# Performance work log

Measured on AMD Instinct MI355X. Metric: run time of the kernel, lower is better.

## Reference

```python
import jax, jax.numpy as jnp
import numpy as np


def setup_inputs() -> dict:
    key = jax.random.key(0)
    ks = jax.random.split(key, 7)
    B, S, E = 2, 4096, 512
    return {
        "query": jax.random.normal(ks[0], (B, S, E), jnp.float32),
        "key": jax.random.normal(ks[1], (B, S, E), jnp.float32),
        "value": jax.random.normal(ks[2], (B, S, E), jnp.float32),
        "in_proj_weight": jax.random.normal(ks[3], (3 * E, E), jnp.float32) * 0.02,
        "in_proj_bias": jax.random.normal(ks[4], (3 * E,), jnp.float32) * 0.02,
        "out_proj_weight": jax.random.normal(ks[5], (E, E), jnp.float32) * 0.02,
        "out_proj_bias": jax.random.normal(ks[6], (E,), jnp.float32) * 0.02,
        "window_size": 512,
        "stride": 256,
    }


def reference(query, key, value, in_proj_weight, in_proj_bias,
              out_proj_weight, out_proj_bias, window_size, stride):
    B, S, E = query.shape
    H = 8
    hd = E // H
    scale = 1.0 / np.sqrt(hd).astype(np.float32)

    # Project full sequences once (equivalent to projecting each window slice).
    wq, wk, wv = in_proj_weight[:E], in_proj_weight[E:2 * E], in_proj_weight[2 * E:]
    bq, bk, bv = in_proj_bias[:E], in_proj_bias[E:2 * E], in_proj_bias[2 * E:]
    qp = query @ wq.T + bq   # [B,S,E]
    kp = key @ wk.T + bk
    vp = value @ wv.T + bv

    # Overlapping window gather: [nw, W] token indices.
    starts = np.arange(0, S - window_size + 1, stride)
    idx = starts[:, None] + np.arange(window_size)[None, :]  # [nw, W]
    nw, W = idx.shape

    def heads(x):  # [B,S,E] -> [B,nw,W,H,hd]
        return x[:, idx].reshape(B, nw, W, H, hd)

    qh, kh, vh = heads(qp), heads(kp), heads(vp)

    scores = jnp.einsum('bnqhd,bnkhd->bnhqk', qh, kh) * scale  # [B,nw,H,W,W]
    probs = jax.nn.softmax(scores, axis=-1)
    ctx = jnp.einsum('bnhqk,bnkhd->bnqhd', probs, vh)           # [B,nw,W,H,hd]
    ctx = ctx.reshape(B, nw * W, E)                             # concat over windows
    return ctx @ out_proj_weight.T + out_proj_bias              # [B, nw*W, E]
```

## Files before the change

### kernel.cpp

```cpp
#include <hip/hip_runtime.h>
#include <hip/hip_bf16.h>

typedef __bf16 bf16x8 __attribute__((ext_vector_type(8)));
typedef float f32x4 __attribute__((ext_vector_type(4)));
typedef float f32x16 __attribute__((ext_vector_type(16)));

__device__ __forceinline__ ushort f2bf(float f) {
  union { float f; unsigned u; } x; x.f = f;
  unsigned r = x.u + 0x7fffu + ((x.u >> 16) & 1u);
  return (ushort)(r >> 16);
}

__device__ __forceinline__ void gld_lds16(const void* g, void* l) {
  __builtin_amdgcn_global_load_lds(
      (const __attribute__((address_space(1))) void*)g,
      (__attribute__((address_space(3))) void*)l, 16, 0, 0);
}

__global__ __launch_bounds__(256) void k_cvt_all(
    const float* __restrict__ q, const float* __restrict__ k,
    const float* __restrict__ v, const float* __restrict__ wi,
    const float* __restrict__ wo, ushort* __restrict__ dst) {
  const int NQ = 1048576;
  const int NWI = 196608, NWO = 65536;
  const int total = 3 * NQ + NWI + NWO;
  int i = blockIdx.x * 256 + threadIdx.x;
  int stride = gridDim.x * 256;
  for (; i < total; i += stride) {
    const float* s; int j;
    if (i < NQ)              { s = q;  j = i; }
    else if (i < 2 * NQ)     { s = k;  j = i - NQ; }
    else if (i < 3 * NQ)     { s = v;  j = i - 2 * NQ; }
    else if (i < 3 * NQ + NWI) { s = wi; j = i - 3 * NQ; }
    else                     { s = wo; j = i - 3 * NQ - NWI; }
    float4 val = reinterpret_cast<const float4*>(s)[j];
    ushort4 o;
    o.x = f2bf(val.x); o.y = f2bf(val.y); o.z = f2bf(val.z); o.w = f2bf(val.w);
    reinterpret_cast<ushort4*>(dst)[i] = o;
  }
}

#define GK 512
#define GN 512

__global__ __launch_bounds__(256) void k_gemm(
    const ushort* __restrict__ Abase, size_t az,
    const ushort* __restrict__ Btbase, size_t bz,
    const float* __restrict__ biasbase, int biz,
    void* __restrict__ Cbase, size_t cz,
    int out_bf16, float qs)
{
  int z = blockIdx.z;
  const ushort* A  = Abase  + az * z;
  const ushort* Bt = Btbase + bz * z;
  const float* bias = biasbase + (size_t)biz * z;
  float osc = (z == 0) ? qs : 1.0f;

  __shared__ ushort As[128 * 32];
  __shared__ ushort Bs[128 * 32];

  int tid = threadIdx.x;
  int wv = tid >> 6, ln = tid & 63;
  int l15 = ln & 15, lg = ln >> 4;
  int wm = wv >> 1, wn = wv & 1;
  int m0 = blockIdx.x * 128, n0 = blockIdx.y * 128;

  f32x4 acc[4][4] = {};

  for (int kt = 0; kt < GK / 32; ++kt) {
    __syncthreads();
#pragma unroll
    for (int h2 = 0; h2 < 2; ++h2) {
      int c = h2 * 256 + wv * 64 + ln;
      int row = c >> 2, kc = (c & 3) * 8;
      gld_lds16(A  + (size_t)(m0 + row) * GK + kt * 32 + kc,
                (char*)As + (h2 * 256 + wv * 64) * 16);
      gld_lds16(Bt + (size_t)(n0 + row) * GK + kt * 32 + kc,
                (char*)Bs + (h2 * 256 + wv * 64) * 16);
    }
    __syncthreads();
    bf16x8 af[4], bf[4];
#pragma unroll
    for (int mf = 0; mf < 4; ++mf)
      af[mf] = *reinterpret_cast<const bf16x8*>(&As[(wm * 64 + mf * 16 + l15) * 32 + lg * 8]);
#pragma unroll
    for (int nf = 0; nf < 4; ++nf)
      bf[nf] = *reinterpret_cast<const bf16x8*>(&Bs[(wn * 64 + nf * 16 + l15) * 32 + lg * 8]);
#pragma unroll
    for (int mf = 0; mf < 4; ++mf)
#pragma unroll
      for (int nf = 0; nf < 4; ++nf)
        acc[mf][nf] = __builtin_amdgcn_mfma_f32_16x16x32_bf16(af[mf], bf[nf], acc[mf][nf], 0, 0, 0);
  }

#pragma unroll
  for (int mf = 0; mf < 4; ++mf)
#pragma unroll
    for (int nf = 0; nf < 4; ++nf)
#pragma unroll
      for (int r = 0; r < 4; ++r) {
        int rr = m0 + wm * 64 + mf * 16 + lg * 4 + r;
        int cc = n0 + wn * 64 + nf * 16 + l15;
        float v = (acc[mf][nf][r] + bias[cc]) * osc;
        if (out_bf16)
          ((ushort*)Cbase + cz * z)[(size_t)rr * GN + cc] = f2bf(v);
        else
          ((float*)Cbase)[(size_t)rr * GN + cc] = v;
      }
}

__global__ __launch_bounds__(512, 4) void k_attn(
    const ushort* __restrict__ qp, const ushort* __restrict__ kp,
    const ushort* __restrict__ vp, ushort* __restrict__ ctx)
{
  const int E = 512, SEQ = 4096;
  int bid = blockIdx.x;
  int qh = bid & 1;
  int h = (bid >> 1) & 7;
  int n = (bid >> 4) % 15;
  int b = bid / 240;
  int start = n * 256;

  int tid = threadIdx.x;
  int w = tid >> 6, ln = tid & 63;
  int l31 = ln & 31, hi = ln >> 5;

  size_t base = ((size_t)(b * SEQ + start)) * E + h * 64;
  const ushort* Kw = kp + base;
  const ushort* Vw = vp + base;
  const ushort* Qw = qp + base;

  __shared__ ushort Vt[32768];

  {
    const ushort* src = Vw + (size_t)tid * E;
    uint4 rowv[8];
#pragma unroll
    for (int i = 0; i < 8; ++i)
      rowv[i] = reinterpret_cast<const uint4*>(src)[i];
    const uint* rw = (const uint*)rowv;
    char* lbw = (char*)Vt;
    int kb2 = tid * 2;
#pragma unroll
    for (int d = 0; d < 64; ++d) {
      uint vv = rw[d >> 1];
      ushort e = (d & 1) ? (ushort)(vv >> 16) : (ushort)(vv & 0xffffu);
      int off = d * 1024 + (kb2 ^ ((d & 7) << 4));
      *(ushort*)(lbw + off) = e;
    }
  }
  __syncthreads();

  int q0 = qh * 256 + w * 32;

  bf16x8 qf[4];
#pragma unroll
  for (int i = 0; i < 4; ++i)
    qf[i] = *reinterpret_cast<const bf16x8*>(
        Qw + (size_t)(q0 + l31) * E + i * 16 + hi * 8);

  f32x16 c0 = {}, c1 = {};
  float psum = 0.f;
  const char* lb = (const char*)Vt;

#pragma unroll 2
  for (int kb = 0; kb < 16; ++kb) {
    bf16x8 kf[4];
#pragma unroll
    for (int i = 0; i < 4; ++i)
      kf[i] = *reinterpret_cast<const bf16x8*>(
          Kw + (size_t)(kb * 32 + l31) * E + i * 16 + hi * 8);

    f32x16 s = {};
    __builtin_amdgcn_s_setprio(1);
#pragma unroll
    for (int i = 0; i < 4; ++i)
      s = __builtin_amdgcn_mfma_f32_32x32x16_bf16(kf[i], qf[i], s, 0, 0, 0);
    __builtin_amdgcn_s_setprio(0);

#pragma unroll
    for (int r = 0; r < 16; ++r) {
      float e = __builtin_amdgcn_exp2f(s[r]);
      s[r] = e;
      psum += e;
    }

    uint cw[8];
#pragma unroll
    for (int i = 0; i < 8; ++i)
      asm("v_cvt_pk_bf16_f32 %0, %1, %2"
          : "=v"(cw[i]) : "v"(s[2 * i]), "v"(s[2 * i + 1]));
    asm volatile("v_permlane32_swap_b32 %0, %1" : "+v"(cw[0]), "+v"(cw[2]));
    asm volatile("v_permlane32_swap_b32 %0, %1" : "+v"(cw[1]), "+v"(cw[3]));
    asm volatile("v_permlane32_swap_b32 %0, %1" : "+v"(cw[4]), "+v"(cw[6]));
    asm volatile("v_permlane32_swap_b32 %0, %1" : "+v"(cw[5]), "+v"(cw[7]));
    union { uint u[4]; bf16x8 v; } A1, A2;
    A1.u[0] = cw[0]; A1.u[1] = cw[1]; A1.u[2] = cw[2]; A1.u[3] = cw[3];
    A2.u[0] = cw[4]; A2.u[1] = cw[5]; A2.u[2] = cw[6]; A2.u[3] = cw[7];

    bf16x8 vb00, vb01, vb10, vb11;
    {
      int row = l31, rowh = 32 + l31;
      int cb0 = kb * 64 + hi * 16;
      int cb1 = cb0 + 32;
      vb00 = *reinterpret_cast<const bf16x8*>(lb + row * 1024 + (cb0 ^ ((row & 7) << 4)));
      vb01 = *reinterpret_cast<const bf16x8*>(lb + rowh * 1024 + (cb0 ^ ((row & 7) << 4)));
      vb10 = *reinterpret_cast<const bf16x8*>(lb + row * 1024 + (cb1 ^ ((row & 7) << 4)));
      vb11 = *reinterpret_cast<const bf16x8*>(lb + rowh * 1024 + (cb1 ^ ((row & 7) << 4)));
    }
    __builtin_amdgcn_s_setprio(1);
    c0 = __builtin_amdgcn_mfma_f32_32x32x16_bf16(A1.v, vb00, c0, 0, 0, 0);
    c1 = __builtin_amdgcn_mfma_f32_32x32x16_bf16(A1.v, vb01, c1, 0, 0, 0);
    c0 = __builtin_amdgcn_mfma_f32_32x32x16_bf16(A2.v, vb10, c0, 0, 0, 0);
    c1 = __builtin_amdgcn_mfma_f32_32x32x16_bf16(A2.v, vb11, c1, 0, 0, 0);
    __builtin_amdgcn_s_setprio(0);
  }

  psum += __shfl_xor(psum, 32);
  float rinv_me = 1.0f / psum;
  size_t orow0 = (size_t)b * 7680 + (size_t)n * 512 + q0;
#pragma unroll
  for (int r = 0; r < 16; ++r) {
    int qrel = (r & 3) + 8 * (r >> 2) + 4 * hi;
    float ri = __shfl(rinv_me, qrel);
    ushort* dst = ctx + (orow0 + qrel) * E + h * 64 + l31;
    dst[0]  = f2bf(c0[r] * ri);
    dst[32] = f2bf(c1[r] * ri);
  }
}

extern "C" void kernel_launch(void* const* d_in, const int* in_sizes, int n_in,
                              void* d_out, int out_size, void* d_ws, size_t ws_size,
                              hipStream_t stream) {
  const float* query = (const float*)d_in[0];
  const float* key   = (const float*)d_in[1];
  const float* value = (const float*)d_in[2];
  const float* ipw   = (const float*)d_in[3];
  const float* ipb   = (const float*)d_in[4];
  const float* opw   = (const float*)d_in[5];
  const float* opb   = (const float*)d_in[6];

  ushort* qb  = (ushort*)d_ws;
  ushort* kb  = qb  + 4194304;
  ushort* vb  = kb  + 4194304;
  ushort* wib = vb  + 4194304;
  ushort* wob = wib + 786432;
  ushort* qp  = wob + 262144;
  ushort* kp  = qp  + 4194304;
  ushort* vp  = kp  + 4194304;
  ushort* ctx = vp  + 4194304;

  const float SC = 0.125f * 1.44269504088896340736f;

  k_cvt_all<<<2048, 256, 0, stream>>>(query, key, value, ipw, opw, qb);

  k_gemm<<<dim3(64, 4, 3), 256, 0, stream>>>(
      qb, (size_t)4194304, wib, (size_t)262144, ipb, 512,
      (void*)qp, (size_t)4194304, 1, SC);

  k_attn<<<480, 512, 0, stream>>>(qp, kp, vp, ctx);

  k_gemm<<<dim3(120, 4, 1), 256, 0, stream>>>(
      ctx, (size_t)0, wob, (size_t)0, opb, 0,
      d_out, (size_t)0, 0, 1.0f);
}
```

Measured before the change: 95.22 us.

## Split attention blocks into quarter-query tiles with two-phase V staging

The attention kernel now launches 960 blocks of 256 threads instead of 480 blocks of 512. Each block handles 128 queries, and block ids are remapped so the 8 blocks sharing a window and head are spread apart. V is transposed into a half-size 32KB LDS buffer in two 256-key phases separated by barriers, using packed 4-key 8-byte stores instead of per-element 2-byte stores. Smaller LDS per block and smaller blocks aim to raise occupancy and improve load balance across CUs. The cost is that K/V for each window-head is re-read by twice as many blocks, and there are extra barriers between phases.

```diff
diff --git a/kernel.cpp b/kernel.cpp
--- a/kernel.cpp
+++ b/kernel.cpp
@@ -109,16 +109,17 @@
       }
 }
 
-__global__ __launch_bounds__(512, 4) void k_attn(
+__global__ __launch_bounds__(256, 4) void k_attn(
     const ushort* __restrict__ qp, const ushort* __restrict__ kp,
     const ushort* __restrict__ vp, ushort* __restrict__ ctx)
 {
   const int E = 512, SEQ = 4096;
-  int bid = blockIdx.x;
-  int qh = bid & 1;
-  int h = (bid >> 1) & 7;
-  int n = (bid >> 4) % 15;
-  int b = bid / 240;
+  int bid0 = blockIdx.x;
+  int bid = (bid0 & 7) * 120 + (bid0 >> 3);
+  int qq = bid & 3;
+  int h = (bid >> 2) & 7;
+  int n = (bid >> 5) % 15;
+  int b = bid / 480;
   int start = n * 256;
 
   int tid = threadIdx.x;
@@ -130,91 +131,119 @@
   const ushort* Vw = vp + base;
   const ushort* Qw = qp + base;
 
-  __shared__ ushort Vt[32768];
-
+  __shared__ ushort Vt[16384];
+
+  int q0 = qq * 128 + w * 32;
+
+  bf16x8 qf0, qf1, qf2, qf3;
   {
-    const ushort* src = Vw + (size_t)tid * E;
-    uint4 rowv[8];
-#pragma unroll
-    for (int i = 0; i < 8; ++i)
-      rowv[i] = reinterpret_cast<const uint4*>(src)[i];
-    const uint* rw = (const uint*)rowv;
-    char* lbw = (char*)Vt;
-    int kb2 = tid * 2;
-#pragma unroll
-    for (int d = 0; d < 64; ++d) {
-      uint vv = rw[d >> 1];
-      ushort e = (d & 1) ? (ushort)(vv >> 16) : (ushort)(vv & 0xffffu);
-      int off = d * 1024 + (kb2 ^ ((d & 7) << 4));
-      *(ushort*)(lbw + off) = e;
-    }
-  }
-  __syncthreads();
-
-  int q0 = qh * 256 + w * 32;
-
-  bf16x8 qf[4];
-#pragma unroll
-  for (int i = 0; i < 4; ++i)
-    qf[i] = *reinterpret_cast<const bf16x8*>(
-        Qw + (size_t)(q0 + l31) * E + i * 16 + hi * 8);
+    const ushort* qr = Qw + (size_t)(q0 + l31) * E + hi * 8;
+    qf0 = *reinterpret_cast<const bf16x8*>(qr + 0);
+    qf1 = *reinterpret_cast<const bf16x8*>(qr + 16);
+    qf2 = *reinterpret_cast<const bf16x8*>(qr + 32);
+    qf3 = *reinterpret_cast<const bf16x8*>(qr + 48);
+  }
 
   f32x16 c0 = {}, c1 = {};
   float psum = 0.f;
   const char* lb = (const char*)Vt;
 
-#pragma unroll 2
-  for (int kb = 0; kb < 16; ++kb) {
-    bf16x8 kf[4];
-#pragma unroll
-    for (int i = 0; i < 4; ++i)
-      kf[i] = *reinterpret_cast<const bf16x8*>(
-          Kw + (size_t)(kb * 32 + l31) * E + i * 16 + hi * 8);
-
-    f32x16 s = {};
-    __builtin_amdgcn_s_setprio(1);
-#pragma unroll
-    for (int i = 0; i < 4; ++i)
-      s = __builtin_amdgcn_mfma_f32_32x32x16_bf16(kf[i], qf[i], s, 0, 0, 0);
-    __builtin_amdgcn_s_setprio(0);
-
-#pragma unroll
-    for (int r = 0; r < 16; ++r) {
-      float e = __builtin_amdgcn_exp2f(s[r]);
-      s[r] = e;
-      psum += e;
-    }
-
-    uint cw[8];
-#pragma unroll
-    for (int i = 0; i < 8; ++i)
-      asm("v_cvt_pk_bf16_f32 %0, %1, %2"
-          : "=v"(cw[i]) : "v"(s[2 * i]), "v"(s[2 * i + 1]));
-    asm volatile("v_permlane32_swap_b32 %0, %1" : "+v"(cw[0]), "+v"(cw[2]));
-    asm volatile("v_permlane32_swap_b32 %0, %1" : "+v"(cw[1]), "+v"(cw[3]));
-    asm volatile("v_permlane32_swap_b32 %0, %1" : "+v"(cw[4]), "+v"(cw[6]));
-    asm volatile("v_permlane32_swap_b32 %0, %1" : "+v"(cw[5]), "+v"(cw[7]));
-    union { uint u[4]; bf16x8 v; } A1, A2;
-    A1.u[0] = cw[0]; A1.u[1] = cw[1]; A1.u[2] = cw[2]; A1.u[3] = cw[3];
-    A2.u[0] = cw[4]; A2.u[1] = cw[5]; A2.u[2] = cw[6]; A2.u[3] = cw[7];
-
-    bf16x8 vb00, vb01, vb10, vb11;
-    {
-      int row = l31, rowh = 32 + l31;
-      int cb0 = kb * 64 + hi * 16;
-      int cb1 = cb0 + 32;
-      vb00 = *reinterpret_cast<const bf16x8*>(lb + row * 1024 + (cb0 ^ ((row & 7) << 4)));
-      vb01 = *reinterpret_cast<const bf16x8*>(lb + rowh * 1024 + (cb0 ^ ((row & 7) << 4)));
-      vb10 = *reinterpret_cast<const bf16x8*>(lb + row * 1024 + (cb1 ^ ((row & 7) << 4)));
-      vb11 = *reinterpret_cast<const bf16x8*>(lb + rowh * 1024 + (cb1 ^ ((row & 7) << 4)));
-    }
-    __builtin_amdgcn_s_setprio(1);
-    c0 = __builtin_amdgcn_mfma_f32_32x32x16_bf16(A1.v, vb00, c0, 0, 0, 0);
-    c1 = __builtin_amdgcn_mfma_f32_32x32x16_bf16(A1.v, vb01, c1, 0, 0, 0);
-    c0 = __builtin_amdgcn_mfma_f32_32x32x16_bf16(A2.v, vb10, c0, 0, 0, 0);
-    c1 = __builtin_amdgcn_mfma_f32_32x32x16_bf16(A2.v, vb11, c1, 0, 0, 0);
-    __builtin_amdgcn_s_setprio(0);
-  }
+  int sk = (tid & 63) * 4;
+  int sd = (tid >> 6) * 16;
+
+#define STAGE_V(G)                                                            \
+  {                                                                           \
+    const ushort* src = Vw + (size_t)((G) * 256 + sk) * E + sd;               \
+    union { uint4 q[2]; ushort u[16]; } R0, R1, R2, R3;                       \
+    R0.q[0] = *(const uint4*)(src);         R0.q[1] = *(const uint4*)(src + 8);         \
+    R1.q[0] = *(const uint4*)(src + E);     R1.q[1] = *(const uint4*)(src + E + 8);     \
+    R2.q[0] = *(const uint4*)(src + 2 * E); R2.q[1] = *(const uint4*)(src + 2 * E + 8); \
+    R3.q[0] = *(const uint4*)(src + 3 * E); R3.q[1] = *(const uint4*)(src + 3 * E + 8); \
+    _Pragma("unroll")                                                         \
+    for (int d0 = 0; d0 < 16; ++d0) {                                         \
+      int d = sd + d0;                                                        \
+      uint2 val;                                                              \
+      val.x = (uint)R0.u[d0] | ((uint)R1.u[d0] << 16);                        \
+      val.y = (uint)R2.u[d0] | ((uint)R3.u[d0] << 16);                        \
+      int off = d * 512 + ((sk * 2) ^ ((d & 7) << 4));                        \
+      *(uint2*)((char*)Vt + off) = val;                                       \
+    }                                                                         \
+  }
+
+#define ATTN_BODY(KB, G)                                                      \
+  {                                                                           \
+    bf16x8 kf0, kf1, kf2, kf3;                                                \
+    {                                                                         \
+      const ushort* kr = Kw + (size_t)(((G) * 8 + (KB)) * 32 + l31) * E + hi * 8; \
+      kf0 = *reinterpret_cast<const bf16x8*>(kr + 0);                         \
+      kf1 = *reinterpret_cast<const bf16x8*>(kr + 16);                        \
+      kf2 = *reinterpret_cast<const bf16x8*>(kr + 32);                        \
+      kf3 = *reinterpret_cast<const bf16x8*>(kr + 48);                        \
+    }                                                                         \
+    bf16x8 vb00, vb01, vb10, vb11;                                            \
+    {                                                                         \
+      int row = l31, rowh = 32 + l31;                                         \
+      int cb0 = (KB) * 64 + hi * 16;                                          \
+      int cb1 = cb0 + 32;                                                     \
+      int xr = (row & 7) << 4;                                                \
+      vb00 = *reinterpret_cast<const bf16x8*>(lb + row * 512 + (cb0 ^ xr));   \
+      vb01 = *reinterpret_cast<const bf16x8*>(lb + rowh * 512 + (cb0 ^ xr));  \
+      vb10 = *reinterpret_cast<const bf16x8*>(lb + row * 512 + (cb1 ^ xr));   \
+      vb11 = *reinterpret_cast<const bf16x8*>(lb + rowh * 512 + (cb1 ^ xr));  \
+    }                                                                         \
+    f32x16 s = {};                                                            \
+    __builtin_amdgcn_s_setprio(1);                                            \
+    s = __builtin_amdgcn_mfma_f32_32x32x16_bf16(kf0, qf0, s, 0, 0, 0);        \
+    s = __builtin_amdgcn_mfma_f32_32x32x16_bf16(kf1, qf1, s, 0, 0, 0);        \
+    s = __builtin_amdgcn_mfma_f32_32x32x16_bf16(kf2, qf2, s, 0, 0, 0);        \
+    s = __builtin_amdgcn_mfma_f32_32x32x16_bf16(kf3, qf3, s, 0, 0, 0);        \
+    __builtin_amdgcn_s_setprio(0);                                            \
+    _Pragma("unroll")                                                         \
+    for (int r = 0; r < 16; ++r)                                              \
+      s[r] = __builtin_amdgcn_exp2f(s[r]);                                    \
+    {                                                                         \
+      float t0 = (s[0] + s[1]) + (s[2] + s[3]);                               \
+      float t1 = (s[4] + s[5]) + (s[6] + s[7]);                               \
+      float t2 = (s[8] + s[9]) + (s[10] + s[11]);                             \
+      float t3 = (s[12] + s[13]) + (s[14] + s[15]);                           \
+      psum += (t0 + t1) + (t2 + t3);                                          \
+    }                                                                         \
+    uint cw0, cw1, cw2, cw3, cw4, cw5, cw6, cw7;                              \
+    asm("v_cvt_pk_bf16_f32 %0, %1, %2" : "=v"(cw0) : "v"(s[0]),  "v"(s[1]));  \
+    asm("v_cvt_pk_bf16_f32 %0, %1, %2" : "=v"(cw1) : "v"(s[2]),  "v"(s[3]));  \
+    asm("v_cvt_pk_bf16_f32 %0, %1, %2" : "=v"(cw2) : "v"(s[4]),  "v"(s[5]));  \
+    asm("v_cvt_pk_bf16_f32 %0, %1, %2" : "=v"(cw3) : "v"(s[6]),  "v"(s[7]));  \
+    asm("v_cvt_pk_bf16_f32 %0, %1, %2" : "=v"(cw4) : "v"(s[8]),  "v"(s[9]));  \
+    asm("v_cvt_pk_bf16_f32 %0, %1, %2" : "=v"(cw5) : "v"(s[10]), "v"(s[11])); \
+    asm("v_cvt_pk_bf16_f32 %0, %1, %2" : "=v"(cw6) : "v"(s[12]), "v"(s[13])); \
+    asm("v_cvt_pk_bf16_f32 %0, %1, %2" : "=v"(cw7) : "v"(s[14]), "v"(s[15])); \
+    asm("v_permlane32_swap_b32 %0, %1" : "+v"(cw0), "+v"(cw2));               \
+    asm("v_permlane32_swap_b32 %0, %1" : "+v"(cw1), "+v"(cw3));               \
+    asm("v_permlane32_swap_b32 %0, %1" : "+v"(cw4), "+v"(cw6));               \
+    asm("v_permlane32_swap_b32 %0, %1" : "+v"(cw5), "+v"(cw7));               \
+    union { uint u[4]; bf16x8 v; } A1, A2;                                    \
+    A1.u[0] = cw0; A1.u[1] = cw1; A1.u[2] = cw2; A1.u[3] = cw3;               \
+    A2.u[0] = cw4; A2.u[1] = cw5; A2.u[2] = cw6; A2.u[3] = cw7;               \
+    __builtin_amdgcn_s_setprio(1);                                            \
+    c0 = __builtin_amdgcn_mfma_f32_32x32x16_bf16(A1.v, vb00, c0, 0, 0, 0);    \
+    c1 = __builtin_amdgcn_mfma_f32_32x32x16_bf16(A1.v, vb01, c1, 0, 0, 0);    \
+    c0 = __builtin_amdgcn_mfma_f32_32x32x16_bf16(A2.v, vb10, c0, 0, 0, 0);    \
+    c1 = __builtin_amdgcn_mfma_f32_32x32x16_bf16(A2.v, vb11, c1, 0, 0, 0);    \
+    __builtin_amdgcn_s_setprio(0);                                            \
+  }
+
+  STAGE_V(0);
+  __syncthreads();
+#pragma unroll
+  for (int kb = 0; kb < 8; ++kb) ATTN_BODY(kb, 0);
+  __syncthreads();
+  STAGE_V(1);
+  __syncthreads();
+#pragma unroll
+  for (int kb = 0; kb < 8; ++kb) ATTN_BODY(kb, 1);
+
+#undef STAGE_V
+#undef ATTN_BODY
 
   psum += __shfl_xor(psum, 32);
   float rinv_me = 1.0f / psum;
@@ -258,7 +287,7 @@
       qb, (size_t)4194304, wib, (size_t)262144, ipb, 512,
       (void*)qp, (size_t)4194304, 1, SC);
 
-  k_attn<<<480, 512, 0, stream>>>(qp, kp, vp, ctx);
+  k_attn<<<960, 256, 0, stream>>>(qp, kp, vp, ctx);
 
   k_gemm<<<dim3(120, 4, 1), 256, 0, stream>>>(
       ctx, (size_t)0, wob, (size_t)0, opb, 0,
```

Result: slower. 106.3 us (+11.6%).

## Process two query tiles per wave in attention to reuse K and V fragments

Applied to the files above, without the earlier changes.

The attention kernel drops to 256 threads per block, and each wave now handles 64 query rows as two 32-row tiles. Each K fragment load and each V LDS read therefore feeds twice as many MFMAs, roughly halving K global traffic per query. The V transpose into LDS now writes 16-byte vectors built from 8 rows instead of scalar shorts, and block IDs are remapped so neighbouring blocks spread across XCDs. The cost is higher register pressure and fewer waves per block, which may reduce latency hiding.

```diff
diff --git a/kernel.cpp b/kernel.cpp
--- a/kernel.cpp
+++ b/kernel.cpp
@@ -109,12 +109,13 @@
       }
 }
 
-__global__ __launch_bounds__(512, 4) void k_attn(
+__global__ __launch_bounds__(256, 2) void k_attn(
     const ushort* __restrict__ qp, const ushort* __restrict__ kp,
     const ushort* __restrict__ vp, ushort* __restrict__ ctx)
 {
   const int E = 512, SEQ = 4096;
-  int bid = blockIdx.x;
+  int bid0 = blockIdx.x;
+  int bid = (bid0 & 7) * 60 + (bid0 >> 3);
   int qh = bid & 1;
   int h = (bid >> 1) & 7;
   int n = (bid >> 4) % 15;
@@ -133,99 +134,163 @@
   __shared__ ushort Vt[32768];
 
   {
-    const ushort* src = Vw + (size_t)tid * E;
-    uint4 rowv[8];
-#pragma unroll
-    for (int i = 0; i < 8; ++i)
-      rowv[i] = reinterpret_cast<const uint4*>(src)[i];
-    const uint* rw = (const uint*)rowv;
-    char* lbw = (char*)Vt;
-    int kb2 = tid * 2;
-#pragma unroll
-    for (int d = 0; d < 64; ++d) {
-      uint vv = rw[d >> 1];
-      ushort e = (d & 1) ? (ushort)(vv >> 16) : (ushort)(vv & 0xffffu);
-      int off = d * 1024 + (kb2 ^ ((d & 7) << 4));
-      *(ushort*)(lbw + off) = e;
+    int sk = (tid & 63) * 8;
+    int sd = (tid >> 6) * 16;
+    const ushort* src = Vw + (size_t)sk * E + sd;
+    union { uint4 q[2]; ushort u[16]; } R0, R1, R2, R3, R4, R5, R6, R7;
+    R0.q[0] = *(const uint4*)(src + 0 * E); R0.q[1] = *(const uint4*)(src + 0 * E + 8);
+    R1.q[0] = *(const uint4*)(src + 1 * E); R1.q[1] = *(const uint4*)(src + 1 * E + 8);
+    R2.q[0] = *(const uint4*)(src + 2 * E); R2.q[1] = *(const uint4*)(src + 2 * E + 8);
+    R3.q[0] = *(const uint4*)(src + 3 * E); R3.q[1] = *(const uint4*)(src + 3 * E + 8);
+    R4.q[0] = *(const uint4*)(src + 4 * E); R4.q[1] = *(const uint4*)(src + 4 * E + 8);
+    R5.q[0] = *(const uint4*)(src + 5 * E); R5.q[1] = *(const uint4*)(src + 5 * E + 8);
+    R6.q[0] = *(const uint4*)(src + 6 * E); R6.q[1] = *(const uint4*)(src + 6 * E + 8);
+    R7.q[0] = *(const uint4*)(src + 7 * E); R7.q[1] = *(const uint4*)(src + 7 * E + 8);
+#pragma unroll
+    for (int d0 = 0; d0 < 16; ++d0) {
+      int d = sd + d0;
+      uint4 val;
+      val.x = (uint)R0.u[d0] | ((uint)R1.u[d0] << 16);
+      val.y = (uint)R2.u[d0] | ((uint)R3.u[d0] << 16);
+      val.z = (uint)R4.u[d0] | ((uint)R5.u[d0] << 16);
+      val.w = (uint)R6.u[d0] | ((uint)R7.u[d0] << 16);
+      int off = d * 1024 + ((sk * 2) ^ ((d & 7) << 4));
+      *(uint4*)((char*)Vt + off) = val;
     }
   }
   __syncthreads();
 
-  int q0 = qh * 256 + w * 32;
-
-  bf16x8 qf[4];
-#pragma unroll
-  for (int i = 0; i < 4; ++i)
-    qf[i] = *reinterpret_cast<const bf16x8*>(
-        Qw + (size_t)(q0 + l31) * E + i * 16 + hi * 8);
-
-  f32x16 c0 = {}, c1 = {};
-  float psum = 0.f;
+  int q0 = qh * 256 + w * 64;
+
+  bf16x8 qa0, qa1, qa2, qa3, qb0, qb1, qb2, qb3;
+  {
+    const ushort* qra = Qw + (size_t)(q0 + l31) * E + hi * 8;
+    const ushort* qrb = qra + (size_t)32 * E;
+    qa0 = *reinterpret_cast<const bf16x8*>(qra + 0);
+    qa1 = *reinterpret_cast<const bf16x8*>(qra + 16);
+    qa2 = *reinterpret_cast<const bf16x8*>(qra + 32);
+    qa3 = *reinterpret_cast<const bf16x8*>(qra + 48);
+    qb0 = *reinterpret_cast<const bf16x8*>(qrb + 0);
+    qb1 = *reinterpret_cast<const bf16x8*>(qrb + 16);
+    qb2 = *reinterpret_cast<const bf16x8*>(qrb + 32);
+    qb3 = *reinterpret_cast<const bf16x8*>(qrb + 48);
+  }
+
+  f32x16 ca0 = {}, ca1 = {}, cb0_ = {}, cb1_ = {};
+  float psa = 0.f, psb = 0.f;
   const char* lb = (const char*)Vt;
 
-#pragma unroll 2
+#pragma unroll
   for (int kb = 0; kb < 16; ++kb) {
-    bf16x8 kf[4];
-#pragma unroll
-    for (int i = 0; i < 4; ++i)
-      kf[i] = *reinterpret_cast<const bf16x8*>(
-          Kw + (size_t)(kb * 32 + l31) * E + i * 16 + hi * 8);
-
-    f32x16 s = {};
-    __builtin_amdgcn_s_setprio(1);
-#pragma unroll
-    for (int i = 0; i < 4; ++i)
-      s = __builtin_amdgcn_mfma_f32_32x32x16_bf16(kf[i], qf[i], s, 0, 0, 0);
-    __builtin_amdgcn_s_setprio(0);
-
-#pragma unroll
-    for (int r = 0; r < 16; ++r) {
-      float e = __builtin_amdgcn_exp2f(s[r]);
-      s[r] = e;
-      psum += e;
-    }
-
-    uint cw[8];
-#pragma unroll
-    for (int i = 0; i < 8; ++i)
-      asm("v_cvt_pk_bf16_f32 %0, %1, %2"
-          : "=v"(cw[i]) : "v"(s[2 * i]), "v"(s[2 * i + 1]));
-    asm volatile("v_permlane32_swap_b32 %0, %1" : "+v"(cw[0]), "+v"(cw[2]));
-    asm volatile("v_permlane32_swap_b32 %0, %1" : "+v"(cw[1]), "+v"(cw[3]));
-    asm volatile("v_permlane32_swap_b32 %0, %1" : "+v"(cw[4]), "+v"(cw[6]));
-    asm volatile("v_permlane32_swap_b32 %0, %1" : "+v"(cw[5]), "+v"(cw[7]));
-    union { uint u[4]; bf16x8 v; } A1, A2;
-    A1.u[0] = cw[0]; A1.u[1] = cw[1]; A1.u[2] = cw[2]; A1.u[3] = cw[3];
-    A2.u[0] = cw[4]; A2.u[1] = cw[5]; A2.u[2] = cw[6]; A2.u[3] = cw[7];
-
+    bf16x8 kf0, kf1, kf2, kf3;
+    {
+      const ushort* kr = Kw + (size_t)(kb * 32 + l31) * E + hi * 8;
+      kf0 = *reinterpret_cast<const bf16x8*>(kr + 0);
+      kf1 = *reinterpret_cast<const bf16x8*>(kr + 16);
+      kf2 = *reinterpret_cast<const bf16x8*>(kr + 32);
+      kf3 = *reinterpret_cast<const bf16x8*>(kr + 48);
+    }
     bf16x8 vb00, vb01, vb10, vb11;
     {
       int row = l31, rowh = 32 + l31;
       int cb0 = kb * 64 + hi * 16;
       int cb1 = cb0 + 32;
-      vb00 = *reinterpret_cast<const bf16x8*>(lb + row * 1024 + (cb0 ^ ((row & 7) << 4)));
-      vb01 = *reinterpret_cast<const bf16x8*>(lb + rowh * 1024 + (cb0 ^ ((row & 7) << 4)));
-      vb10 = *reinterpret_cast<const bf16x8*>(lb + row * 1024 + (cb1 ^ ((row & 7) << 4)));
-      vb11 = *reinterpret_cast<const bf16x8*>(lb + rowh * 1024 + (cb1 ^ ((row & 7) << 4)));
-    }
+      int xr0 = (row & 7) << 4;
+      vb00 = *reinterpret_cast<const bf16x8*>(lb + row * 1024 + (cb0 ^ xr0));
+      vb01 = *reinterpret_cast<const bf16x8*>(lb + rowh * 1024 + (cb0 ^ xr0));
+      vb10 = *reinterpret_cast<const bf16x8*>(lb + row * 1024 + (cb1 ^ xr0));
+      vb11 = *reinterpret_cast<const bf16x8*>(lb + rowh * 1024 + (cb1 ^ xr0));
+    }
+
+    f32x16 s1 = {}, s2 = {};
     __builtin_amdgcn_s_setprio(1);
-    c0 = __builtin_amdgcn_mfma_f32_32x32x16_bf16(A1.v, vb00, c0, 0, 0, 0);
-    c1 = __builtin_amdgcn_mfma_f32_32x32x16_bf16(A1.v, vb01, c1, 0, 0, 0);
-    c0 = __builtin_amdgcn_mfma_f32_32x32x16_bf16(A2.v, vb10, c0, 0, 0, 0);
-    c1 = __builtin_amdgcn_mfma_f32_32x32x16_bf16(A2.v, vb11, c1, 0, 0, 0);
+    s1 = __builtin_amdgcn_mfma_f32_32x32x16_bf16(kf0, qa0, s1, 0, 0, 0);
+    s2 = __builtin_amdgcn_mfma_f32_32x32x16_bf16(kf0, qb0, s2, 0, 0, 0);
+    s1 = __builtin_amdgcn_mfma_f32_32x32x16_bf16(kf1, qa1, s1, 0, 0, 0);
+    s2 = __builtin_amdgcn_mfma_f32_32x32x16_bf16(kf1, qb1, s2, 0, 0, 0);
+    s1 = __builtin_amdgcn_mfma_f32_32x32x16_bf16(kf2, qa2, s1, 0, 0, 0);
+    s2 = __builtin_amdgcn_mfma_f32_32x32x16_bf16(kf2, qb2, s2, 0, 0, 0);
+    s1 = __builtin_amdgcn_mfma_f32_32x32x16_bf16(kf3, qa3, s1, 0, 0, 0);
+    s2 = __builtin_amdgcn_mfma_f32_32x32x16_bf16(kf3, qb3, s2, 0, 0, 0);
     __builtin_amdgcn_s_setprio(0);
-  }
-
-  psum += __shfl_xor(psum, 32);
-  float rinv_me = 1.0f / psum;
+
+#pragma unroll
+    for (int r = 0; r < 16; ++r) s1[r] = __builtin_amdgcn_exp2f(s1[r]);
+#pragma unroll
+    for (int r = 0; r < 16; ++r) s2[r] = __builtin_amdgcn_exp2f(s2[r]);
+    {
+      float t0 = (s1[0] + s1[1]) + (s1[2] + s1[3]);
+      float t1 = (s1[4] + s1[5]) + (s1[6] + s1[7]);
+      float t2 = (s1[8] + s1[9]) + (s1[10] + s1[11]);
+      float t3 = (s1[12] + s1[13]) + (s1[14] + s1[15]);
+      psa += (t0 + t1) + (t2 + t3);
+      float u0 = (s2[0] + s2[1]) + (s2[2] + s2[3]);
+      float u1 = (s2[4] + s2[5]) + (s2[6] + s2[7]);
+      float u2 = (s2[8] + s2[9]) + (s2[10] + s2[11]);
+      float u3 = (s2[12] + s2[13]) + (s2[14] + s2[15]);
+      psb += (u0 + u1) + (u2 + u3);
+    }
+
+    uint a0, a1, a2, a3, a4, a5, a6, a7;
+    asm("v_cvt_pk_bf16_f32 %0, %1, %2" : "=v"(a0) : "v"(s1[0]),  "v"(s1[1]));
+    asm("v_cvt_pk_bf16_f32 %0, %1, %2" : "=v"(a1) : "v"(s1[2]),  "v"(s1[3]));
+    asm("v_cvt_pk_bf16_f32 %0, %1, %2" : "=v"(a2) : "v"(s1[4]),  "v"(s1[5]));
+    asm("v_cvt_pk_bf16_f32 %0, %1, %2" : "=v"(a3) : "v"(s1[6]),  "v"(s1[7]));
+    asm("v_cvt_pk_bf16_f32 %0, %1, %2" : "=v"(a4) : "v"(s1[8]),  "v"(s1[9]));
+    asm("v_cvt_pk_bf16_f32 %0, %1, %2" : "=v"(a5) : "v"(s1[10]), "v"(s1[11]));
+    asm("v_cvt_pk_bf16_f32 %0, %1, %2" : "=v"(a6) : "v"(s1[12]), "v"(s1[13]));
+    asm("v_cvt_pk_bf16_f32 %0, %1, %2" : "=v"(a7) : "v"(s1[14]), "v"(s1[15]));
+    asm("v_permlane32_swap_b32 %0, %1" : "+v"(a0), "+v"(a2));
+    asm("v_permlane32_swap_b32 %0, %1" : "+v"(a1), "+v"(a3));
+    asm("v_permlane32_swap_b32 %0, %1" : "+v"(a4), "+v"(a6));
+    asm("v_permlane32_swap_b32 %0, %1" : "+v"(a5), "+v"(a7));
+    uint b0, b1, b2, b3, b4, b5, b6, b7;
+    asm("v_cvt_pk_bf16_f32 %0, %1, %2" : "=v"(b0) : "v"(s2[0]),  "v"(s2[1]));
+    asm("v_cvt_pk_bf16_f32 %0, %1, %2" : "=v"(b1) : "v"(s2[2]),  "v"(s2[3]));
+    asm("v_cvt_pk_bf16_f32 %0, %1, %2" : "=v"(b2) : "v"(s2[4]),  "v"(s2[5]));
+    asm("v_cvt_pk_bf16_f32 %0, %1, %2" : "=v"(b3) : "v"(s2[6]),  "v"(s2[7]));
+    asm("v_cvt_pk_bf16_f32 %0, %1, %2" : "=v"(b4) : "v"(s2[8]),  "v"(s2[9]));
+    asm("v_cvt_pk_bf16_f32 %0, %1, %2" : "=v"(b5) : "v"(s2[10]), "v"(s2[11]));
+    asm("v_cvt_pk_bf16_f32 %0, %1, %2" : "=v"(b6) : "v"(s2[12]), "v"(s2[13]));
+    asm("v_cvt_pk_bf16_f32 %0, %1, %2" : "=v"(b7) : "v"(s2[14]), "v"(s2[15]));
+    asm("v_permlane32_swap_b32 %0, %1" : "+v"(b0), "+v"(b2));
+    asm("v_permlane32_swap_b32 %0, %1" : "+v"(b1), "+v"(b3));
+    asm("v_permlane32_swap_b32 %0, %1" : "+v"(b4), "+v"(b6));
+    asm("v_permlane32_swap_b32 %0, %1" : "+v"(b5), "+v"(b7));
+    union { uint u[4]; bf16x8 v; } A1, A2, B1, B2;
+    A1.u[0] = a0; A1.u[1] = a1; A1.u[2] = a2; A1.u[3] = a3;
+    A2.u[0] = a4; A2.u[1] = a5; A2.u[2] = a6; A2.u[3] = a7;
+    B1.u[0] = b0; B1.u[1] = b1; B1.u[2] = b2; B1.u[3] = b3;
+    B2.u[0] = b4; B2.u[1] = b5; B2.u[2] = b6; B2.u[3] = b7;
+
+    __builtin_amdgcn_s_setprio(1);
+    ca0  = __builtin_amdgcn_mfma_f32_32x32x16_bf16(A1.v, vb00, ca0, 0, 0, 0);
+    cb0_ = __builtin_amdgcn_mfma_f32_32x32x16_bf16(B1.v, vb00, cb0_, 0, 0, 0);
+    ca1  = __builtin_amdgcn_mfma_f32_32x32x16_bf16(A1.v, vb01, ca1, 0, 0, 0);
+    cb1_ = __builtin_amdgcn_mfma_f32_32x32x16_bf16(B1.v, vb01, cb1_, 0, 0, 0);
+    ca0  = __builtin_amdgcn_mfma_f32_32x32x16_bf16(A2.v, vb10, ca0, 0, 0, 0);
+    cb0_ = __builtin_amdgcn_mfma_f32_32x32x16_bf16(B2.v, vb10, cb0_, 0, 0, 0);
+    ca1  = __builtin_amdgcn_mfma_f32_32x32x16_bf16(A2.v, vb11, ca1, 0, 0, 0);
+    cb1_ = __builtin_amdgcn_mfma_f32_32x32x16_bf16(B2.v, vb11, cb1_, 0, 0, 0);
+    __builtin_amdgcn_s_setprio(0);
+  }
+
+  psa += __shfl_xor(psa, 32);
+  psb += __shfl_xor(psb, 32);
+  float ria = 1.0f / psa;
+  float rib = 1.0f / psb;
   size_t orow0 = (size_t)b * 7680 + (size_t)n * 512 + q0;
 #pragma unroll
   for (int r = 0; r < 16; ++r) {
     int qrel = (r & 3) + 8 * (r >> 2) + 4 * hi;
-    float ri = __shfl(rinv_me, qrel);
-    ushort* dst = ctx + (orow0 + qrel) * E + h * 64 + l31;
-    dst[0]  = f2bf(c0[r] * ri);
-    dst[32] = f2bf(c1[r] * ri);
+    float r1 = __shfl(ria, qrel);
+    float r2 = __shfl(rib, qrel);
+    ushort* dA = ctx + (orow0 + qrel) * E + h * 64 + l31;
+    ushort* dB = ctx + (orow0 + 32 + qrel) * E + h * 64 + l31;
+    dA[0]  = f2bf(ca0[r] * r1);
+    dA[32] = f2bf(ca1[r] * r1);
+    dB[0]  = f2bf(cb0_[r] * r2);
+    dB[32] = f2bf(cb1_[r] * r2);
   }
 }
 
@@ -258,7 +323,7 @@
       qb, (size_t)4194304, wib, (size_t)262144, ipb, 512,
       (void*)qp, (size_t)4194304, 1, SC);
 
-  k_attn<<<480, 512, 0, stream>>>(qp, kp, vp, ctx);
+  k_attn<<<480, 256, 0, stream>>>(qp, kp, vp, ctx);
 
   k_gemm<<<dim3(120, 4, 1), 256, 0, stream>>>(
       ctx, (size_t)0, wob, (size_t)0, opb, 0,
```

Result: faster. 87.75 us (-7.8%).
